# Optimization experiments

Measured on AMD Instinct MI355X. Metric: run time of the kernel, lower is better.

## Reference

```python
import jax, jax.numpy as jnp
import numpy as np

OUT_H = 7
OUT_W = 7
RATIO = 2  # sampling_ratio (static)


def _roi_align(feat, boxes, out_h, out_w, sx, sy, ratio):
    """torchvision-style RoIAlign (aligned=False) on a single image.
    feat: [C,H,W], boxes: [N,4] (x1,y1,x2,y2) in image coords.
    sx, sy: spatial scales (W_feat/W_img, H_feat/H_img). Returns [N,C,out_h,out_w]."""
    C, H, W = feat.shape
    N = boxes.shape[0]
    x1 = boxes[:, 0] * sx
    y1 = boxes[:, 1] * sy
    x2 = boxes[:, 2] * sx
    y2 = boxes[:, 3] * sy
    rw = jnp.maximum(x2 - x1, 1.0)
    rh = jnp.maximum(y2 - y1, 1.0)
    bw = rw / out_w
    bh = rh / out_h
    offs = (jnp.arange(ratio, dtype=feat.dtype) + 0.5) / ratio  # sub-bin sample offsets
    # sample coordinates: [N, out*ratio]
    gy = y1[:, None, None] + (jnp.arange(out_h, dtype=feat.dtype)[None, :, None] + offs[None, None, :]) * bh[:, None, None]
    gx = x1[:, None, None] + (jnp.arange(out_w, dtype=feat.dtype)[None, :, None] + offs[None, None, :]) * bw[:, None, None]
    Y = gy.reshape(N, out_h * ratio)
    X = gx.reshape(N, out_w * ratio)
    vy = (Y >= -1.0) & (Y <= H)
    vx = (X >= -1.0) & (X <= W)
    Yc = jnp.clip(Y, 0.0, H - 1)
    Xc = jnp.clip(X, 0.0, W - 1)
    y0 = jnp.floor(Yc).astype(jnp.int32)
    x0 = jnp.floor(Xc).astype(jnp.int32)
    y1i = jnp.minimum(y0 + 1, H - 1)
    x1i = jnp.minimum(x0 + 1, W - 1)
    ly = Yc - y0.astype(Yc.dtype)
    lx = Xc - x0.astype(Xc.dtype)
    hy = 1.0 - ly
    hx = 1.0 - lx

    def g(yi, xi):  # corner gather -> [C, N, out_h*ratio, out_w*ratio]
        return feat[:, yi[:, :, None], xi[:, None, :]]

    val = (hy[:, :, None] * hx[:, None, :]) * g(y0, x0) \
        + (hy[:, :, None] * lx[:, None, :]) * g(y0, x1i) \
        + (ly[:, :, None] * hx[:, None, :]) * g(y1i, x0) \
        + (ly[:, :, None] * lx[:, None, :]) * g(y1i, x1i)
    valid = vy[:, :, None] & vx[:, None, :]
    val = jnp.where(valid[None], val, 0.0)
    # average over the ratio x ratio sampling grid (always divide by ratio^2)
    val = val.reshape(C, N, out_h, ratio, out_w, ratio).mean(axis=(3, 5))
    return val.transpose(1, 0, 2, 3)


def setup_inputs() -> dict:
    key = jax.random.key(0)
    k0, k1, k2, kb = jax.random.split(key, 4)
    img_h, img_w = 800, 1216
    feat0 = jax.random.normal(k0, (1, 256, 200, 304), dtype=jnp.float32)
    feat1 = jax.random.normal(k1, (1, 256, 100, 152), dtype=jnp.float32)
    feat2 = jax.random.normal(k2, (1, 256, 50, 76), dtype=jnp.float32)
    u = jax.random.uniform(kb, (256, 4), dtype=jnp.float32)
    bx1 = u[:, 0] * (img_w - 32)
    by1 = u[:, 1] * (img_h - 32)
    bw = 16.0 + u[:, 2] * 256.0
    bh = 16.0 + u[:, 3] * 256.0
    bx2 = jnp.minimum(bx1 + bw, float(img_w))
    by2 = jnp.minimum(by1 + bh, float(img_h))
    boxes = jnp.stack([bx1, by1, bx2, by2], axis=1)
    return {"feat0": feat0, "feat1": feat1, "feat2": feat2, "boxes": boxes,
            "img_h": img_h, "img_w": img_w}


def reference(feat0, feat1, feat2, boxes, img_h, img_w):
    _, C, H, W = feat0.shape
    # upsample coarser levels by 2**i, half-pixel bilinear == torch align_corners=False
    ups = [feat0]
    for i, f in enumerate([feat1, feat2], 1):
        s = 2 ** i
        ups.append(jax.image.resize(
            f, (f.shape[0], f.shape[1], f.shape[2] * s, f.shape[3] * s), method='bilinear'))
    fused = jnp.concatenate(ups, axis=1)[0]  # [3C, H, W] (single image)
    sx = W / img_w
    sy = H / img_h
    return _roi_align(fused, boxes, OUT_H, OUT_W, sx, sy, RATIO)
```

## Files before the change

kernel.cpp:

```cpp
#include <hip/hip_runtime.h>
#include <hip/hip_bf16.h>

#define H0 200
#define W0 304
#define H1 100
#define W1 152
#define H2 50
#define W2 76
#define CPL 256
#define CTOT 768
#define OH 7
#define OW 7
#define NPOS 49

#define P0 (H0*W0)
#define P1 (H1*W1)
#define P2 (H2*W2)
#define T0_OFF ((size_t)0)
#define T1_OFF ((size_t)P0*CPL)
#define T2_OFF ((size_t)P0*CPL + (size_t)P1*CPL)
#define WS_ELEMS ((size_t)P0*CPL + (size_t)P1*CPL + (size_t)P2*CPL)
#define WS_BYTES (WS_ELEMS * 2)

__device__ __forceinline__ float hat01(float d) {
    return fmaxf(0.0f, 1.0f - fabsf(d));
}

__device__ __forceinline__ unsigned short f2bf_rne(float x) {
    unsigned int u = __float_as_uint(x);
    u += 0x7fffu + ((u >> 16) & 1u);
    return (unsigned short)(u >> 16);
}

__global__ void __launch_bounds__(256)
transpose_all_kernel(const float* __restrict__ f0, const float* __restrict__ f1,
                     const float* __restrict__ f2,
                     unsigned short* __restrict__ T0,
                     unsigned short* __restrict__ T1,
                     unsigned short* __restrict__ T2, int n0, int n01) {
    __shared__ unsigned short tile[64][72];
    int b = blockIdx.x;
    const float* in; unsigned short* outp; int P; int rel;
    if (b < n0)       { in = f0; outp = T0; P = P0; rel = b; }
    else if (b < n01) { in = f1; outp = T1; P = P1; rel = b - n0; }
    else              { in = f2; outp = T2; P = P2; rel = b - n01; }
    int p0 = (rel >> 2) * 64;
    int c0 = (rel & 3) * 64;

    int q = threadIdx.x & 15;
    int r = threadIdx.x >> 4;
    bool full = (p0 + 64 <= P);
#pragma unroll
    for (int i = 0; i < 4; ++i) {
        int c = c0 + r + 16 * i;
        int p = p0 + 4 * q;
        float4 v;
        if (full) {
            v = *(const float4*)(in + (size_t)c * P + p);
        } else {
            v.x = (p + 0 < P) ? in[(size_t)c * P + p + 0] : 0.0f;
            v.y = (p + 1 < P) ? in[(size_t)c * P + p + 1] : 0.0f;
            v.z = (p + 2 < P) ? in[(size_t)c * P + p + 2] : 0.0f;
            v.w = (p + 3 < P) ? in[(size_t)c * P + p + 3] : 0.0f;
        }
        tile[4 * q + 0][r + 16 * i] = f2bf_rne(v.x);
        tile[4 * q + 1][r + 16 * i] = f2bf_rne(v.y);
        tile[4 * q + 2][r + 16 * i] = f2bf_rne(v.z);
        tile[4 * q + 3][r + 16 * i] = f2bf_rne(v.w);
    }
    __syncthreads();
#pragma unroll
    for (int i = 0; i < 4; ++i) {
        int p = p0 + r + 16 * i;
        if (p < P) {
            ushort4 w = *(const ushort4*)&tile[r + 16 * i][4 * q];
            *(ushort4*)(outp + (size_t)p * CPL + c0 + 4 * q) = w;
        }
    }
}

template<int TY, int TX>
__device__ __forceinline__ float4 accum_pos(const unsigned short* __restrict__ Tc,
                                            const int* yi, const float* yw,
                                            const int* xi, const float* xw) {
    float a0 = 0.0f, a1 = 0.0f, a2 = 0.0f, a3 = 0.0f;
#pragma unroll
    for (int a = 0; a < TY; ++a) {
        float s0 = 0.0f, s1 = 0.0f, s2 = 0.0f, s3 = 0.0f;
#pragma unroll
        for (int b = 0; b < TX; ++b) {
            uint2 v = *(const uint2*)(Tc + (unsigned)(yi[a] + xi[b]));
            float wxb = xw[b];
            s0 += wxb * __uint_as_float(v.x << 16);
            s1 += wxb * __uint_as_float(v.x & 0xffff0000u);
            s2 += wxb * __uint_as_float(v.y << 16);
            s3 += wxb * __uint_as_float(v.y & 0xffff0000u);
        }
        a0 += yw[a] * s0; a1 += yw[a] * s1; a2 += yw[a] * s2; a3 += yw[a] * s3;
    }
    float4 r;
    r.x = a0 * 0.25f; r.y = a1 * 0.25f; r.z = a2 * 0.25f; r.w = a3 * 0.25f;
    return r;
}

template<int TY, int TX>
__device__ __forceinline__ void run_level(const unsigned short* __restrict__ Tc,
                                          const int (*s_idx)[6], const float (*s_w)[6],
                                          float (*sout)[260], int wv, int coff) {
    for (int pos = wv; pos < NPOS; pos += 8) {
        int oh = pos / 7;
        int ow = pos - oh * 7;
        int yi[6], xi[6];
        float yw[6], xw[6];
#pragma unroll
        for (int j = 0; j < 6; ++j) {
            yi[j] = s_idx[oh][j];     yw[j] = s_w[oh][j];
            xi[j] = s_idx[7 + ow][j]; xw[j] = s_w[7 + ow][j];
        }
        float4 res = accum_pos<TY, TX>(Tc, yi, yw, xi, xw);
        *(float4*)&sout[pos][coff] = res;
    }
}

__global__ void __launch_bounds__(512)
roi_align_cl4_kernel(const unsigned short* __restrict__ T0,
                     const unsigned short* __restrict__ T1,
                     const unsigned short* __restrict__ T2,
                     const float* __restrict__ boxes,
                     const int* __restrict__ img_h_p,
                     const int* __restrict__ img_w_p,
                     float* __restrict__ out) {
    __shared__ float sout[NPOS][260];
    __shared__ int   s_idx[14][6];
    __shared__ float s_w[14][6];

    int n = blockIdx.x;
    int level = blockIdx.y;
    const unsigned short* T; int Hc, Wc; float inv_s;
    if (level == 0)      { T = T0; Hc = H0; Wc = W0; inv_s = 1.0f;  }
    else if (level == 1) { T = T1; Hc = H1; Wc = W1; inv_s = 0.5f;  }
    else                 { T = T2; Hc = H2; Wc = W2; inv_s = 0.25f; }

    int tid = threadIdx.x;
    if (tid < 14) {
        int axis = (tid >= 7) ? 1 : 0;
        int o = tid - axis * 7;
        float sx = (float)W0 / (float)img_w_p[0];
        float sy = (float)H0 / (float)img_h_p[0];
        float a1, bs; int Hf, Hca, mul;
        if (axis) {
            a1 = boxes[n * 4 + 0] * sx;
            float a2 = boxes[n * 4 + 2] * sx;
            bs = fmaxf(a2 - a1, 1.0f) * (1.0f / (float)OW);
            Hf = W0; Hca = Wc; mul = 1;
        } else {
            a1 = boxes[n * 4 + 1] * sy;
            float a2 = boxes[n * 4 + 3] * sy;
            bs = fmaxf(a2 - a1, 1.0f) * (1.0f / (float)OH);
            Hf = H0; Hca = Hc; mul = Wc;
        }
        int idx[6]; float w[6];
#pragma unroll
        for (int j = 0; j < 6; ++j) { idx[j] = 0; w[j] = 0.0f; }
        if (level == 0) {
#pragma unroll
            for (int r2 = 0; r2 < 2; ++r2) {
                float Y = a1 + ((float)o + 0.25f + 0.5f * (float)r2) * bs;
                float v = (Y >= -1.0f && Y <= (float)Hf) ? 1.0f : 0.0f;
                float Yc = fminf(fmaxf(Y, 0.0f), (float)(Hf - 1));
                int y0 = (int)Yc; float lf = Yc - (float)y0;
                idx[2 * r2]     = y0;                  w[2 * r2]     = (1.0f - lf) * v;
                idx[2 * r2 + 1] = min(y0 + 1, Hf - 1); w[2 * r2 + 1] = lf * v;
            }
        } else {
            int bases[2]; float w3[2][3];
#pragma unroll
            for (int r2 = 0; r2 < 2; ++r2) {
                float Y = a1 + ((float)o + 0.25f + 0.5f * (float)r2) * bs;
                float v = (Y >= -1.0f && Y <= (float)Hf) ? 1.0f : 0.0f;
                float Yc = fminf(fmaxf(Y, 0.0f), (float)(Hf - 1));
                int y0 = (int)Yc; float lf = Yc - (float)y0; float hf = 1.0f - lf;
                int yf1 = min(y0 + 1, Hf - 1);
                float yc0 = fminf(fmaxf(((float)y0 + 0.5f) * inv_s - 0.5f, 0.0f), (float)(Hca - 1));
                float yc1 = fminf(fmaxf(((float)yf1 + 0.5f) * inv_s - 0.5f, 0.0f), (float)(Hca - 1));
                int b2 = (int)yc0;
                bases[r2] = b2;
#pragma unroll
                for (int t2 = 0; t2 < 3; ++t2) {
                    float j2 = (float)(b2 + t2);
                    w3[r2][t2] = v * (hf * hat01(yc0 - j2) + lf * hat01(yc1 - j2));
                }
            }
            int dmax = (level == 1) ? 3 : 2;
            int d = min(max(bases[1] - bases[0], 0), dmax);
            w[0] += w3[0][0]; w[1] += w3[0][1]; w[2] += w3[0][2];
            w[d] += w3[1][0]; w[d + 1] += w3[1][1]; w[d + 2] += w3[1][2];
#pragma unroll
            for (int j = 0; j < 6; ++j) idx[j] = min(bases[0] + j, Hca - 1);
        }
#pragma unroll
        for (int j = 0; j < 6; ++j) { s_idx[tid][j] = idx[j] * mul * CPL; s_w[tid][j] = w[j]; }
    }
    __syncthreads();

    int lane = tid & 63;
    int wv = tid >> 6;
    int coff = lane * 4;
    const unsigned short* Tc = T + coff;

    if (level == 0)      run_level<4, 4>(Tc, s_idx, s_w, sout, wv, coff);
    else if (level == 1) run_level<6, 6>(Tc, s_idx, s_w, sout, wv, coff);
    else                 run_level<5, 5>(Tc, s_idx, s_w, sout, wv, coff);
    __syncthreads();

    size_t obase = ((size_t)n * CTOT + (size_t)level * CPL) * NPOS;
    for (int i2 = tid; i2 < CPL * NPOS; i2 += 512) {
        int c = i2 / NPOS;
        int p = i2 - c * NPOS;
        out[obase + i2] = sout[p][c];
    }
}

__device__ __forceinline__ void axis_w3_fb(int yf0, int Hf, int Hc, float inv_s,
                                           float lf, int& base, float* w) {
    int yf1 = min(yf0 + 1, Hf - 1);
    float hf = 1.0f - lf;
    float yc0 = fminf(fmaxf(((float)yf0 + 0.5f) * inv_s - 0.5f, 0.0f), (float)(Hc - 1));
    float yc1 = fminf(fmaxf(((float)yf1 + 0.5f) * inv_s - 0.5f, 0.0f), (float)(Hc - 1));
    base = (int)yc0;
#pragma unroll
    for (int r = 0; r < 3; ++r) {
        float j = (float)(base + r);
        w[r] = hf * hat01(yc0 - j) + lf * hat01(yc1 - j);
    }
}

__global__ void __launch_bounds__(256)
roi_align_fused_fb_kernel(const float* __restrict__ f0,
                          const float* __restrict__ f1,
                          const float* __restrict__ f2,
                          const float* __restrict__ boxes,
                          const int* __restrict__ img_h_p,
                          const int* __restrict__ img_w_p,
                          float* __restrict__ out,
                          int total) {
    int i = blockIdx.x * blockDim.x + threadIdx.x;
    if (i >= total) return;
    int ow = i % OW;
    int t = i / OW;
    int oh = t % OH; t /= OH;
    int c = t % CTOT;
    int n = t / CTOT;
    float sx = (float)W0 / (float)img_w_p[0];
    float sy = (float)H0 / (float)img_h_p[0];
    float bx1 = boxes[n * 4 + 0] * sx;
    float by1 = boxes[n * 4 + 1] * sy;
    float bw = fmaxf(boxes[n * 4 + 2] * sx - bx1, 1.0f) / OW;
    float bh = fmaxf(boxes[n * 4 + 3] * sy - by1, 1.0f) / OH;
    int level = c >> 8;
    int cl = c & (CPL - 1);
    const float* f;
    int Hc, Wc; float inv_s;
    if (level == 0)      { f = f0 + (size_t)cl * P0; Hc = H0; Wc = W0; inv_s = 1.0f;  }
    else if (level == 1) { f = f1 + (size_t)cl * P1; Hc = H1; Wc = W1; inv_s = 0.5f;  }
    else                 { f = f2 + (size_t)cl * P2; Hc = H2; Wc = W2; inv_s = 0.25f; }
    float acc = 0.0f;
#pragma unroll
    for (int ry = 0; ry < 2; ++ry) {
        float Y = by1 + ((float)oh + 0.25f + 0.5f * ry) * bh;
        bool vy = (Y >= -1.0f) && (Y <= (float)H0);
        float Yc = fminf(fmaxf(Y, 0.0f), (float)(H0 - 1));
        int y0 = (int)Yc;
        float ly = Yc - (float)y0;
#pragma unroll
        for (int rx = 0; rx < 2; ++rx) {
            float X = bx1 + ((float)ow + 0.25f + 0.5f * rx) * bw;
            bool vx = (X >= -1.0f) && (X <= (float)W0);
            float Xc = fminf(fmaxf(X, 0.0f), (float)(W0 - 1));
            int x0 = (int)Xc;
            float lx = Xc - (float)x0;
            float v;
            if (level == 0) {
                int y1i = min(y0 + 1, H0 - 1), x1i = min(x0 + 1, W0 - 1);
                float hy = 1.0f - ly, hx = 1.0f - lx;
                float v00 = f[y0 * W0 + x0],  v01 = f[y0 * W0 + x1i];
                float v10 = f[y1i * W0 + x0], v11 = f[y1i * W0 + x1i];
                v = hy * (hx * v00 + lx * v01) + ly * (hx * v10 + lx * v11);
            } else {
                int yb, xb; float wy[3], wxl[3];
                axis_w3_fb(y0, H0, Hc, inv_s, ly, yb, wy);
                axis_w3_fb(x0, W0, Wc, inv_s, lx, xb, wxl);
                v = 0.0f;
#pragma unroll
                for (int a = 0; a < 3; ++a) {
                    int row = min(yb + a, Hc - 1) * Wc;
                    float s = 0.0f;
#pragma unroll
                    for (int b = 0; b < 3; ++b)
                        s += wxl[b] * f[row + min(xb + b, Wc - 1)];
                    v += wy[a] * s;
                }
            }
            if (vy && vx) acc += v;
        }
    }
    out[i] = acc * 0.25f;
}

extern "C" void kernel_launch(void* const* d_in, const int* in_sizes, int n_in,
                              void* d_out, int out_size, void* d_ws, size_t ws_size,
                              hipStream_t stream) {
    const float* f0    = (const float*)d_in[0];
    const float* f1    = (const float*)d_in[1];
    const float* f2    = (const float*)d_in[2];
    const float* boxes = (const float*)d_in[3];
    const int* img_h_p = (const int*)d_in[4];
    const int* img_w_p = (const int*)d_in[5];
    float* out = (float*)d_out;
    int N = in_sizes[3] / 4;

    if (ws_size >= WS_BYTES) {
        unsigned short* ws = (unsigned short*)d_ws;
        unsigned short* T0 = ws + T0_OFF;
        unsigned short* T1 = ws + T1_OFF;
        unsigned short* T2 = ws + T2_OFF;
        int n0 = ((P0 + 63) / 64) * 4;
        int n1 = ((P1 + 63) / 64) * 4;
        int n2 = ((P2 + 63) / 64) * 4;
        transpose_all_kernel<<<n0 + n1 + n2, 256, 0, stream>>>(
            f0, f1, f2, T0, T1, T2, n0, n0 + n1);
        roi_align_cl4_kernel<<<dim3(N, 3), 512, 0, stream>>>(
            T0, T1, T2, boxes, img_h_p, img_w_p, out);
    } else {
        int total = N * CTOT * OH * OW;
        roi_align_fused_fb_kernel<<<(total + 255) / 256, 256, 0, stream>>>(
            f0, f1, f2, boxes, img_h_p, img_w_p, out, total);
    }
}
```

Before: 162.8 us.

## Widen gather loads to 16-byte and pair output positions per wavefront

The ROI gather kernel now has each lane load 8 bf16 channels (uint4) instead of 4, with the two half-wavefronts handling two output positions at once. This halves the number of load instructions per sample and roughly halves the position-loop iterations per wave. The transpose kernel's write-back also moves to 16-byte stores. The padded shared row stride changes to 264. The odd position count means one duplicated position (48) is computed redundantly, and register use rises with eight accumulators.

```diff
diff --git a/kernel.cpp b/kernel.cpp
--- a/kernel.cpp
+++ b/kernel.cpp
@@ -12,6 +12,7 @@
 #define OH 7
 #define OW 7
 #define NPOS 49
+#define SROW 264
 
 #define P0 (H0*W0)
 #define P1 (H1*W1)
@@ -69,68 +70,74 @@
         tile[4 * q + 3][r + 16 * i] = f2bf_rne(v.w);
     }
     __syncthreads();
-#pragma unroll
-    for (int i = 0; i < 4; ++i) {
-        int p = p0 + r + 16 * i;
+    int q8 = threadIdx.x & 7;
+    int r8 = threadIdx.x >> 3;
+#pragma unroll
+    for (int i = 0; i < 2; ++i) {
+        int p = p0 + r8 + 32 * i;
         if (p < P) {
-            ushort4 w = *(const ushort4*)&tile[r + 16 * i][4 * q];
-            *(ushort4*)(outp + (size_t)p * CPL + c0 + 4 * q) = w;
+            uint4 w = *(const uint4*)&tile[r8 + 32 * i][8 * q8];
+            *(uint4*)(outp + (size_t)p * CPL + c0 + 8 * q8) = w;
         }
     }
 }
 
 template<int TY, int TX>
-__device__ __forceinline__ float4 accum_pos(const unsigned short* __restrict__ Tc,
-                                            const int* yi, const float* yw,
-                                            const int* xi, const float* xw) {
-    float a0 = 0.0f, a1 = 0.0f, a2 = 0.0f, a3 = 0.0f;
-#pragma unroll
-    for (int a = 0; a < TY; ++a) {
-        float s0 = 0.0f, s1 = 0.0f, s2 = 0.0f, s3 = 0.0f;
-#pragma unroll
-        for (int b = 0; b < TX; ++b) {
-            uint2 v = *(const uint2*)(Tc + (unsigned)(yi[a] + xi[b]));
-            float wxb = xw[b];
-            s0 += wxb * __uint_as_float(v.x << 16);
-            s1 += wxb * __uint_as_float(v.x & 0xffff0000u);
-            s2 += wxb * __uint_as_float(v.y << 16);
-            s3 += wxb * __uint_as_float(v.y & 0xffff0000u);
-        }
-        a0 += yw[a] * s0; a1 += yw[a] * s1; a2 += yw[a] * s2; a3 += yw[a] * s3;
-    }
-    float4 r;
-    r.x = a0 * 0.25f; r.y = a1 * 0.25f; r.z = a2 * 0.25f; r.w = a3 * 0.25f;
-    return r;
-}
-
-template<int TY, int TX>
-__device__ __forceinline__ void run_level(const unsigned short* __restrict__ Tc,
-                                          const int (*s_idx)[6], const float (*s_w)[6],
-                                          float (*sout)[260], int wv, int coff) {
-    for (int pos = wv; pos < NPOS; pos += 8) {
+__device__ __forceinline__ void run_level_pair(const unsigned short* __restrict__ Tc,
+                                               const int (*s_idx)[6], const float (*s_w)[6],
+                                               float (*sout)[SROW], int wv, int half, int l) {
+    for (int pp = wv; pp < 25; pp += 8) {
+        int pos = 2 * pp + half;
+        pos = (pos > NPOS - 1) ? (NPOS - 1) : pos;
         int oh = pos / 7;
         int ow = pos - oh * 7;
-        int yi[6], xi[6];
-        float yw[6], xw[6];
-#pragma unroll
-        for (int j = 0; j < 6; ++j) {
-            yi[j] = s_idx[oh][j];     yw[j] = s_w[oh][j];
-            xi[j] = s_idx[7 + ow][j]; xw[j] = s_w[7 + ow][j];
-        }
-        float4 res = accum_pos<TY, TX>(Tc, yi, yw, xi, xw);
-        *(float4*)&sout[pos][coff] = res;
+        int yi[TY], xi[TX];
+        float yw[TY], xw[TX];
+#pragma unroll
+        for (int j = 0; j < TY; ++j) { yi[j] = s_idx[oh][j];     yw[j] = s_w[oh][j]; }
+#pragma unroll
+        for (int j = 0; j < TX; ++j) { xi[j] = s_idx[7 + ow][j]; xw[j] = s_w[7 + ow][j]; }
+
+        float a0 = 0.f, a1 = 0.f, a2 = 0.f, a3 = 0.f;
+        float a4 = 0.f, a5 = 0.f, a6 = 0.f, a7 = 0.f;
+#pragma unroll
+        for (int a = 0; a < TY; ++a) {
+            float s0 = 0.f, s1 = 0.f, s2 = 0.f, s3 = 0.f;
+            float s4 = 0.f, s5 = 0.f, s6 = 0.f, s7 = 0.f;
+#pragma unroll
+            for (int b = 0; b < TX; ++b) {
+                uint4 v = *(const uint4*)(Tc + (unsigned)(yi[a] + xi[b]));
+                float wxb = xw[b];
+                s0 += wxb * __uint_as_float(v.x << 16);
+                s1 += wxb * __uint_as_float(v.x & 0xffff0000u);
+                s2 += wxb * __uint_as_float(v.y << 16);
+                s3 += wxb * __uint_as_float(v.y & 0xffff0000u);
+                s4 += wxb * __uint_as_float(v.z << 16);
+                s5 += wxb * __uint_as_float(v.z & 0xffff0000u);
+                s6 += wxb * __uint_as_float(v.w << 16);
+                s7 += wxb * __uint_as_float(v.w & 0xffff0000u);
+            }
+            float wya = yw[a];
+            a0 += wya * s0; a1 += wya * s1; a2 += wya * s2; a3 += wya * s3;
+            a4 += wya * s4; a5 += wya * s5; a6 += wya * s6; a7 += wya * s7;
+        }
+        float4 r0, r1;
+        r0.x = a0 * 0.25f; r0.y = a1 * 0.25f; r0.z = a2 * 0.25f; r0.w = a3 * 0.25f;
+        r1.x = a4 * 0.25f; r1.y = a5 * 0.25f; r1.z = a6 * 0.25f; r1.w = a7 * 0.25f;
+        *(float4*)&sout[pos][8 * l + 0] = r0;
+        *(float4*)&sout[pos][8 * l + 4] = r1;
     }
 }
 
 __global__ void __launch_bounds__(512)
-roi_align_cl4_kernel(const unsigned short* __restrict__ T0,
+roi_align_cl7_kernel(const unsigned short* __restrict__ T0,
                      const unsigned short* __restrict__ T1,
                      const unsigned short* __restrict__ T2,
                      const float* __restrict__ boxes,
                      const int* __restrict__ img_h_p,
                      const int* __restrict__ img_w_p,
                      float* __restrict__ out) {
-    __shared__ float sout[NPOS][260];
+    __shared__ float sout[NPOS][SROW];
     __shared__ int   s_idx[14][6];
     __shared__ float s_w[14][6];
 
@@ -205,12 +212,13 @@
 
     int lane = tid & 63;
     int wv = tid >> 6;
-    int coff = lane * 4;
-    const unsigned short* Tc = T + coff;
-
-    if (level == 0)      run_level<4, 4>(Tc, s_idx, s_w, sout, wv, coff);
-    else if (level == 1) run_level<6, 6>(Tc, s_idx, s_w, sout, wv, coff);
-    else                 run_level<5, 5>(Tc, s_idx, s_w, sout, wv, coff);
+    int half = (lane >> 5) & 1;
+    int l = lane & 31;
+    const unsigned short* Tc = T + l * 8;
+
+    if (level == 0)      run_level_pair<4, 4>(Tc, s_idx, s_w, sout, wv, half, l);
+    else if (level == 1) run_level_pair<6, 6>(Tc, s_idx, s_w, sout, wv, half, l);
+    else                 run_level_pair<5, 5>(Tc, s_idx, s_w, sout, wv, half, l);
     __syncthreads();
 
     size_t obase = ((size_t)n * CTOT + (size_t)level * CPL) * NPOS;
@@ -329,7 +337,7 @@
         int n2 = ((P2 + 63) / 64) * 4;
         transpose_all_kernel<<<n0 + n1 + n2, 256, 0, stream>>>(
             f0, f1, f2, T0, T1, T2, n0, n0 + n1);
-        roi_align_cl4_kernel<<<dim3(N, 3), 512, 0, stream>>>(
+        roi_align_cl7_kernel<<<dim3(N, 3), 512, 0, stream>>>(
             T0, T1, T2, boxes, img_h_p, img_w_p, out);
     } else {
         int total = N * CTOT * OH * OW;
```

Result: no change. 160.9 us (-1.1%).
